# Kernel tuning notes

Measured on AMD Instinct MI355X. Metric: run time of the kernel, lower is better.

The kernel has to match this reference:

```python
import jax
import jax.numpy as jnp
import numpy as np

# ---- static config (matches init_kwargs) ----
V_PATCH_NUMS = [1, 2, 3, 4, 5, 6, 8, 10, 13, 16]
SN = len(V_PATCH_NUMS)
BETA = 0.25
RESI = 0.5          # Phi residual ratio
K_PHI = 4           # share_quant_resi -> PhiPartiallyShared with 4 convs
_ticks = np.linspace(1.0 / 3 / K_PHI, 1 - 1.0 / 3 / K_PHI, K_PHI)  # K==4 branch
PHI_IDX = [int(np.argmin(np.abs(_ticks - si / (SN - 1)))) for si in range(SN)]


def _area_matrix(n_in, n_out):
    """Row-stochastic matrix replicating F.interpolate(mode='area') == adaptive_avg_pool (1D)."""
    M = np.zeros((n_out, n_in), np.float32)
    for i in range(n_out):
        s = (i * n_in) // n_out
        e = -((-(i + 1) * n_in) // n_out)  # ceil
        M[i, s:e] = 1.0 / (e - s)
    return M


def _bicubic_matrix(n_in, n_out):
    """1D bicubic (a=-0.75, align_corners=False, border clamp), matching torch F.interpolate."""
    A = -0.75
    M = np.zeros((n_out, n_in), np.float32)
    scale = n_in / n_out
    for i in range(n_out):
        src = (i + 0.5) * scale - 0.5
        f = int(np.floor(src))
        t = src - f
        for k in range(4):           # taps at f-1 .. f+2
            j = f - 1 + k
            d = abs(src - j)
            if d <= 1.0:
                w = (A + 2) * d ** 3 - (A + 3) * d ** 2 + 1.0
            elif d < 2.0:
                w = A * d ** 3 - 5 * A * d ** 2 + 8 * A * d - 4 * A
            else:
                w = 0.0
            M[i, min(max(j, 0), n_in - 1)] += w
    return M


def _phi(h, w, b):
    # Phi: h*(1-r) + conv3x3(h)*r
    conv = jax.lax.conv_general_dilated(
        h, w, window_strides=(1, 1), padding='SAME',
        dimension_numbers=('NCHW', 'OIHW', 'NCHW')) + b[None, :, None, None]
    return h * (1.0 - RESI) + conv * RESI


def setup_inputs() -> dict:
    key = jax.random.key(0)
    k1, k2, k3 = jax.random.split(key, 3)
    B, C, H = 32, 32, 16
    V = 8192
    f_BChw = jax.random.normal(k1, (B, C, H, H), dtype=jnp.float32)
    emb = jax.random.normal(k2, (V, C), dtype=jnp.float32)
    conv_w = jax.random.normal(k3, (K_PHI, C, C, 3, 3), dtype=jnp.float32) * 0.05
    conv_b = jnp.zeros((K_PHI, C), dtype=jnp.float32)
    return {"f_BChw": f_BChw, "emb": emb, "conv_w": conv_w, "conv_b": conv_b}


def reference(f_BChw, emb, conv_w, conv_b):
    B, C, H, W = f_BChw.shape
    dt = f_BChw.dtype
    f_ng = jax.lax.stop_gradient(f_BChw)
    f_rest = f_ng
    f_hat = jnp.zeros_like(f_ng)
    emb_ng = jax.lax.stop_gradient(emb)     # distances use embedding.weight.data
    emb_sq = jnp.sum(emb_ng ** 2, axis=1)   # [V]
    loss = jnp.zeros((), dt)
    for si, pn in enumerate(V_PATCH_NUMS):
        r = jax.lax.stop_gradient(f_rest)
        if si != SN - 1:
            P = jnp.asarray(_area_matrix(H, pn), dt)
            z = jnp.einsum('ph,bchw,qw->bpqc', P, r, P)   # area pool -> [B,pn,pn,C]
        else:
            z = r.transpose(0, 2, 3, 1)
        z_NC = z.reshape(-1, C)
        d = jnp.sum(z_NC ** 2, axis=1, keepdims=True) + emb_sq - 2.0 * (z_NC @ emb_ng.T)
        idx = jnp.argmin(d, axis=1)                        # [B*pn*pn]
        h = jnp.take(emb, idx, axis=0).reshape(B, pn, pn, C).transpose(0, 3, 1, 2)
        if si != SN - 1:
            U = jnp.asarray(_bicubic_matrix(pn, H), dt)
            h = jnp.einsum('hp,bcpq,wq->bchw', U, h, U)    # bicubic upsample
        pi = PHI_IDX[si]
        h = _phi(h, conv_w[pi], conv_b[pi])
        f_hat = f_hat + h
        f_rest = f_rest - h
        loss = loss + BETA * jnp.mean((jax.lax.stop_gradient(f_hat) - f_BChw) ** 2) \
                    + jnp.mean((f_hat - f_ng) ** 2)
    loss = loss / SN
    f_hat_out = jax.lax.stop_gradient(f_hat) - f_ng + f_BChw   # straight-through
    return f_hat_out, loss
```

## Files before the change

### kernel.cpp

```cpp
#include <hip/hip_runtime.h>
#include <math.h>
#include <stdint.h>

#define B_ 32
#define C_ 32
#define H_ 16
#define V_ 8192
#define HW_ 256
#define NELEM (B_*C_*H_*H_)
#define TBYTES 6208
#define TF4    388

typedef short bf16x8 __attribute__((ext_vector_type(8)));
typedef unsigned short u16x8 __attribute__((ext_vector_type(8)));
typedef float f32x4 __attribute__((ext_vector_type(4)));
typedef unsigned long long ull;

__device__ __forceinline__ unsigned int fkey(float f) {
    unsigned int u = __float_as_uint(f);
    return (u & 0x80000000u) ? ~u : (u | 0x80000000u);
}
__device__ __forceinline__ unsigned short f2bf(float x) {
    unsigned int u = __float_as_uint(x);
    unsigned int r = u + 0x7fffu + ((u >> 16) & 1u);
    return (unsigned short)(r >> 16);
}
__device__ __forceinline__ float bf2f(unsigned short h) {
    return __uint_as_float(((unsigned int)h) << 16);
}

__global__ void __launch_bounds__(256) k_init(
    const float* __restrict__ f, const float* __restrict__ emb,
    float* __restrict__ f_rest, float* __restrict__ f_hat,
    char* __restrict__ blob, float* __restrict__ lossAcc)
{
    int i = blockIdx.x*256 + threadIdx.x;
    if (i < NELEM) { float v = f[i]; f_rest[i] = v; f_hat[i] = 0.f; }
    if (i < 512*64) {
        int t = i >> 6, l = i & 63;
        int row = t*16 + (l & 15);
        int k0 = (l >> 4) * 8;
        const float* er = emb + row*C_ + k0;
        u16x8 h0, h1, h2;
        #pragma unroll
        for (int j = 0; j < 8; ++j) {
            float x = -2.f * er[j];
            unsigned short b0 = f2bf(x);  float r1 = x - bf2f(b0);
            unsigned short b1 = f2bf(r1); float r2 = r1 - bf2f(b1);
            unsigned short b2 = f2bf(r2);
            h0[j] = b0; h1[j] = b1; h2[j] = b2;
        }
        char* tb = blob + (size_t)t*TBYTES;
        *(u16x8*)(tb +        l*16) = h0;
        *(u16x8*)(tb + 2048 + l*16) = h1;
        *(u16x8*)(tb + 4096 + l*16) = h2;
        if ((l >> 4) == 0) {
            const float4* e4 = (const float4*)(emb + row*C_);
            float s = 0.f;
            #pragma unroll
            for (int cc = 0; cc < 8; ++cc) {
                float4 ev = e4[cc];
                s += ev.x*ev.x + ev.y*ev.y + ev.z*ev.z + ev.w*ev.w;
            }
            *(float*)(tb + 6144 + (l & 15)*4) = s;
        }
    }
    if (i == 0) lossAcc[0] = 0.f;
}

__global__ void __launch_bounds__(256) k_pool(
    const float* __restrict__ f_rest, unsigned short* __restrict__ zb,
    ull* __restrict__ best, int pn, int N)
{
    int gid = blockIdx.x*256 + threadIdx.x;
    if (gid >= N*C_) return;
    int c = gid & 31;
    int n = gid >> 5;
    if (c == 0) best[n] = ~0ull;
    int pp = pn*pn;
    int b = n / pp;
    int rem = n - b*pp;
    int p = rem / pn;
    int q = rem - p*pn;
    int hs = (p*H_)/pn,  he = ((p+1)*H_ + pn-1)/pn;
    int ws = (q*H_)/pn,  we = ((q+1)*H_ + pn-1)/pn;
    const float* base = f_rest + ((size_t)(b*C_ + c))*HW_;
    float s = 0.f;
    for (int hh = hs; hh < he; ++hh) {
        #pragma unroll 4
        for (int ww = ws; ww < we; ++ww)
            s += base[hh*H_ + ww];
    }
    float inv = (1.f/(float)(he-hs)) * (1.f/(float)(we-ws));
    float x = s * inv;
    unsigned short b0 = f2bf(x);  float r1 = x - bf2f(b0);
    unsigned short b1 = f2bf(r1); float r2 = r1 - bf2f(b1);
    unsigned short b2 = f2bf(r2);
    size_t o = (size_t)n*C_ + c;
    zb[o]          = b0;
    zb[o + 262144] = b1;
    zb[o + 524288] = b2;
}

__global__ void __launch_bounds__(256) k_vqm(
    const float4* __restrict__ blob, const unsigned short* __restrict__ zb,
    ull* __restrict__ best, int N, int lvs)
{
    __shared__ char chunk[8*TBYTES] __attribute__((aligned(16)));
    int tid = threadIdx.x, lane = tid & 63, w = tid >> 6;
    int qb = blockIdx.x >> lvs;
    int vc = blockIdx.x & ((1 << lvs) - 1);
    int tiles_total = 512 >> lvs;
    int t0 = vc * tiles_total;
    int qt0 = qb*8 + w*2;
    int qr = lane & 15, kq = lane >> 4;

    bf16x8 B00, B01, B02, B10, B11, B12;
    {
        size_t r0 = (size_t)(qt0*16 + qr)*C_ + kq*8;
        size_t r1 = r0 + 16*C_;
        B00 = *(const bf16x8*)(zb + r0);
        B01 = *(const bf16x8*)(zb + r0 + 262144);
        B02 = *(const bf16x8*)(zb + r0 + 524288);
        B10 = *(const bf16x8*)(zb + r1);
        B11 = *(const bf16x8*)(zb + r1 + 262144);
        B12 = *(const bf16x8*)(zb + r1 + 524288);
    }

    float dmin0 = __builtin_inff(), dmin1 = __builtin_inff();
    int imin0 = 0, imin1 = 0;

    for (int tc = 0; tc < tiles_total; tc += 8) {
        int S = (tiles_total - tc) < 8 ? (tiles_total - tc) : 8;
        int cnt = S * TF4;
        __syncthreads();
        const float4* src = blob + (size_t)(t0 + tc)*TF4;
        for (int i = tid; i < cnt; i += 256)
            ((float4*)chunk)[i] = src[i];
        __syncthreads();
        for (int t = 0; t < S; ++t) {
            const char* tb = chunk + t*TBYTES;
            bf16x8 A0 = *(const bf16x8*)(tb +        lane*16);
            bf16x8 A1 = *(const bf16x8*)(tb + 2048 + lane*16);
            bf16x8 A2 = *(const bf16x8*)(tb + 4096 + lane*16);
            f32x4 e2v = *(const f32x4*)(tb + 6144 + kq*16);
            f32x4 a0 = e2v, a1 = e2v;
            #define MF(Af, Bf, Cc) Cc = __builtin_amdgcn_mfma_f32_16x16x32_bf16(Af, Bf, Cc, 0, 0, 0)
            MF(A0, B00, a0); MF(A0, B10, a1);
            MF(A1, B00, a0); MF(A1, B10, a1);
            MF(A0, B01, a0); MF(A0, B11, a1);
            MF(A2, B00, a0); MF(A2, B10, a1);
            MF(A1, B01, a0); MF(A1, B11, a1);
            MF(A0, B02, a0); MF(A0, B12, a1);
            MF(A2, B01, a0); MF(A2, B11, a1);
            MF(A1, B02, a0); MF(A1, B12, a1);
            #undef MF
            int cbase = (t0 + tc + t)*16 + kq*4;
            float mt0 = fminf(fminf(a0.x, a0.y), fminf(a0.z, a0.w));
            if (mt0 < dmin0) {
                dmin0 = mt0;
                imin0 = cbase + ((a0.x==mt0) ? 0 : (a0.y==mt0) ? 1 : (a0.z==mt0) ? 2 : 3);
            }
            float mt1 = fminf(fminf(a1.x, a1.y), fminf(a1.z, a1.w));
            if (mt1 < dmin1) {
                dmin1 = mt1;
                imin1 = cbase + ((a1.x==mt1) ? 0 : (a1.y==mt1) ? 1 : (a1.z==mt1) ? 2 : 3);
            }
        }
    }

    ull k0 = ((ull)fkey(dmin0) << 32) | (unsigned int)imin0;
    ull k1 = ((ull)fkey(dmin1) << 32) | (unsigned int)imin1;
    #pragma unroll
    for (int off = 16; off <= 32; off <<= 1) {
        ull o0 = __shfl_xor(k0, off);
        ull o1 = __shfl_xor(k1, off);
        k0 = o0 < k0 ? o0 : k0;
        k1 = o1 < k1 ? o1 : k1;
    }
    if (kq == 0) {
        int q0 = qt0*16 + qr;
        int q1 = q0 + 16;
        if (q0 < N) atomicMin(best + q0, k0);
        if (q1 < N) atomicMin(best + q1, k1);
    }
}

__device__ __forceinline__ void cubic_taps(int i, int pn, float* wt, int* col) {
    double src = ((double)i + 0.5) * ((double)pn / 16.0) - 0.5;
    double fl = floor(src);
    const double A = -0.75;
    #pragma unroll
    for (int k = 0; k < 4; ++k) {
        double j = fl - 1.0 + (double)k;
        double d = fabs(src - j);
        double w;
        if (d <= 1.0)      w = ((A+2.0)*d - (A+3.0))*d*d + 1.0;
        else if (d < 2.0)  w = ((A*d - 5.0*A)*d + 8.0*A)*d - 4.0*A;
        else               w = 0.0;
        wt[k] = (float)w;
        int jj = (int)j;
        col[k] = jj < 0 ? 0 : (jj > pn-1 ? pn-1 : jj);
    }
}

__global__ void __launch_bounds__(256) k_upphi(
    const ull* __restrict__ best,
    const float* __restrict__ emb,
    const float* __restrict__ cw, const float* __restrict__ cb,
    const float* __restrict__ forig,
    float* __restrict__ f_hat, float* __restrict__ f_rest,
    float* __restrict__ lossAcc, int pn)
{
    __shared__ float hup[16][16][33];
    __shared__ float red[4];
    int bi = blockIdx.x >> 3;
    int g  = blockIdx.x & 7;
    int tid = threadIdx.x;
    int h = tid >> 4, w = tid & 15;

    float wh[4]; int th[4];
    float wwt[4]; int tw[4];
    cubic_taps(h, pn, wh, th);
    cubic_taps(w, pn, wwt, tw);

    float acc[32];
    #pragma unroll
    for (int c = 0; c < 32; ++c) acc[c] = 0.f;
    const ull* bptr = best + bi*pn*pn;
    for (int i = 0; i < 4; ++i) {
        if (wh[i] == 0.f) continue;
        for (int j = 0; j < 4; ++j) {
            float wt = wh[i]*wwt[j];
            if (wt == 0.f) continue;
            unsigned int idx = (unsigned int)(bptr[th[i]*pn + tw[j]] & 0xffffffffull);
            const float4* e4 = (const float4*)(emb + (size_t)idx*C_);
            #pragma unroll
            for (int cc = 0; cc < 8; ++cc) {
                float4 ev = e4[cc];
                acc[cc*4+0] = fmaf(wt, ev.x, acc[cc*4+0]);
                acc[cc*4+1] = fmaf(wt, ev.y, acc[cc*4+1]);
                acc[cc*4+2] = fmaf(wt, ev.z, acc[cc*4+2]);
                acc[cc*4+3] = fmaf(wt, ev.w, acc[cc*4+3]);
            }
        }
    }
    #pragma unroll
    for (int c = 0; c < 32; ++c) hup[h][w][c] = acc[c];
    __syncthreads();

    int co0 = g*4;
    float o4[4];
    #pragma unroll
    for (int k = 0; k < 4; ++k) o4[k] = cb[co0+k];
    for (int ci = 0; ci < 32; ++ci) {
        float hv[9];
        #pragma unroll
        for (int dh = 0; dh < 3; ++dh) {
            int hh = h + dh - 1;
            #pragma unroll
            for (int dw = 0; dw < 3; ++dw) {
                int ww2 = w + dw - 1;
                bool ok = (hh >= 0) & (hh < 16) & (ww2 >= 0) & (ww2 < 16);
                hv[dh*3+dw] = ok ? hup[hh & 15][ww2 & 15][ci] : 0.f;
            }
        }
        #pragma unroll
        for (int k = 0; k < 4; ++k) {
            const float* wr = cw + ((size_t)(co0+k)*C_ + ci)*9;
            float s = 0.f;
            #pragma unroll
            for (int p2 = 0; p2 < 9; ++p2) s = fmaf(hv[p2], wr[p2], s);
            o4[k] += s;
        }
    }

    float sq = 0.f;
    #pragma unroll
    for (int k = 0; k < 4; ++k) {
        float hv0 = hup[h][w][co0+k];
        float outv = 0.5f*hv0 + 0.5f*o4[k];
        size_t off = ((size_t)(bi*C_ + co0 + k))*HW_ + h*16 + w;
        float fh = f_hat[off] + outv;
        f_hat[off] = fh;
        f_rest[off] = f_rest[off] - outv;
        float df = fh - forig[off];
        sq = fmaf(df, df, sq);
    }
    #pragma unroll
    for (int o2 = 32; o2 > 0; o2 >>= 1) sq += __shfl_down(sq, o2, 64);
    if ((tid & 63) == 0) red[tid >> 6] = sq;
    __syncthreads();
    if (tid == 0) atomicAdd(lossAcc, (red[0]+red[1])+(red[2]+red[3]));
}

__global__ void __launch_bounds__(256) k_final(
    const float* __restrict__ f_hat, const float* __restrict__ lossAcc,
    float* __restrict__ out)
{
    int i = blockIdx.x*256 + threadIdx.x;
    if (i < NELEM) out[i] = f_hat[i];
    if (i == 0) out[NELEM] = lossAcc[0] * 1.25f / ((float)NELEM * 10.f);
}

extern "C" void kernel_launch(void* const* d_in, const int* in_sizes, int n_in,
                              void* d_out, int out_size, void* d_ws, size_t ws_size,
                              hipStream_t stream)
{
    const float* f   = (const float*)d_in[0];
    const float* emb = (const float*)d_in[1];
    const float* cw  = (const float*)d_in[2];
    const float* cb  = (const float*)d_in[3];
    float* out = (float*)d_out;
    char* ws = (char*)d_ws;
    ull*   best   = (ull*)ws;
    float* f_rest = (float*)(ws + 65536);
    float* f_hat  = (float*)(ws + 65536 + 1048576);
    unsigned short* zb = (unsigned short*)(ws + 2162688);
    char*  blob   = ws + 3735552;
    float* lossAcc = (float*)(ws + 3735552 + 512*TBYTES);

    volatile double a   = 1.0/3.0/4.0;
    volatile double bb  = 1.0 - a;
    volatile double stp = (bb - a) / 3.0;
    double ticks[4];
    for (int i = 0; i < 4; ++i) { volatile double m = (double)i * stp; ticks[i] = m + a; }
    ticks[3] = bb;
    static const int pns[10] = {1,2,3,4,5,6,8,10,13,16};
    int phi_idx[10];
    for (int si = 0; si < 10; ++si) {
        volatile double x = (double)si / 9.0;
        int bi = 0; double bd = fabs(ticks[0] - x);
        for (int k = 1; k < 4; ++k) {
            double d = fabs(ticks[k] - x);
            if (d < bd) { bd = d; bi = k; }
        }
        phi_idx[si] = bi;
    }

    k_init<<<1024, 256, 0, stream>>>(f, emb, f_rest, f_hat, blob, lossAcc);

    static const int lvss[10] = {7,7,7,7,6,6,5,4,4,3};
    for (int si = 0; si < 10; ++si) {
        int pn = pns[si];
        int N = B_*pn*pn;
        int pthr = N*C_;
        k_pool<<<(pthr+255)/256, 256, 0, stream>>>(f_rest, zb, best, pn, N);
        int qtiles = (N + 127)/128;
        int lvs = lvss[si];
        k_vqm<<<qtiles << lvs, 256, 0, stream>>>((const float4*)blob, zb, best, N, lvs);
        const float* cwp = cw + (size_t)phi_idx[si]*C_*C_*9;
        const float* cbp = cb + (size_t)phi_idx[si]*C_;
        k_upphi<<<B_*8, 256, 0, stream>>>(best, emb, cwp, cbp, f, f_hat, f_rest,
                                          lossAcc, pn);
    }
    k_final<<<1024, 256, 0, stream>>>(f_hat, lossAcc, out);
}
```

Measured before the change: 498.1 us.

## Fuse next-scale pooling into upphi and restructure VQ argmin kernel

The area pooling and bf16 split for the next scale now run at the end of k_upphi, using the freshly updated f_rest held in shared memory. This removes the separate k_pool launch per scale, and ping-pong best buffers let each scale reset the next scale's buffer. k_vqm no longer stages codebook tiles through LDS with barriers; it streams them from global memory with register double-buffering, and each wave now handles 4 query tiles instead of 2. The vocab split factors and launch bounds are retuned to match. In exchange, the kernel relies on cache hits for the codebook reads and uses more registers per wave.

```diff
diff --git a/kernel.cpp b/kernel.cpp
--- a/kernel.cpp
+++ b/kernel.cpp
@@ -9,7 +9,7 @@
 #define HW_ 256
 #define NELEM (B_*C_*H_*H_)
 #define TBYTES 6208
-#define TF4    388
+#define ZPL 262144
 
 typedef short bf16x8 __attribute__((ext_vector_type(8)));
 typedef unsigned short u16x8 __attribute__((ext_vector_type(8)));
@@ -86,103 +86,126 @@
     int ws = (q*H_)/pn,  we = ((q+1)*H_ + pn-1)/pn;
     const float* base = f_rest + ((size_t)(b*C_ + c))*HW_;
     float s = 0.f;
-    for (int hh = hs; hh < he; ++hh) {
-        #pragma unroll 4
+    for (int hh = hs; hh < he; ++hh)
         for (int ww = ws; ww < we; ++ww)
             s += base[hh*H_ + ww];
-    }
     float inv = (1.f/(float)(he-hs)) * (1.f/(float)(we-ws));
     float x = s * inv;
     unsigned short b0 = f2bf(x);  float r1 = x - bf2f(b0);
     unsigned short b1 = f2bf(r1); float r2 = r1 - bf2f(b1);
     unsigned short b2 = f2bf(r2);
     size_t o = (size_t)n*C_ + c;
-    zb[o]          = b0;
-    zb[o + 262144] = b1;
-    zb[o + 524288] = b2;
-}
-
-__global__ void __launch_bounds__(256) k_vqm(
-    const float4* __restrict__ blob, const unsigned short* __restrict__ zb,
+    zb[o] = b0; zb[o + ZPL] = b1; zb[o + 2*ZPL] = b2;
+}
+
+__device__ __forceinline__ void qstep(
+    const bf16x8 a0, const bf16x8 a1, const bf16x8 a2, const f32x4 e2v,
+    const bf16x8* Bf, int cbase, float& dmin, int& imin)
+{
+    f32x4 acc = e2v;
+    acc = __builtin_amdgcn_mfma_f32_16x16x32_bf16(a0, Bf[0], acc, 0, 0, 0);
+    acc = __builtin_amdgcn_mfma_f32_16x16x32_bf16(a1, Bf[0], acc, 0, 0, 0);
+    acc = __builtin_amdgcn_mfma_f32_16x16x32_bf16(a0, Bf[1], acc, 0, 0, 0);
+    acc = __builtin_amdgcn_mfma_f32_16x16x32_bf16(a2, Bf[0], acc, 0, 0, 0);
+    acc = __builtin_amdgcn_mfma_f32_16x16x32_bf16(a1, Bf[1], acc, 0, 0, 0);
+    acc = __builtin_amdgcn_mfma_f32_16x16x32_bf16(a0, Bf[2], acc, 0, 0, 0);
+    float mt = fminf(fminf(acc.x, acc.y), fminf(acc.z, acc.w));
+    if (mt < dmin) {
+        dmin = mt;
+        imin = cbase + ((acc.x==mt) ? 0 : (acc.y==mt) ? 1 : (acc.z==mt) ? 2 : 3);
+    }
+}
+
+__global__ void __launch_bounds__(256, 2) k_vqm(
+    const char* __restrict__ blob, const unsigned short* __restrict__ zb,
     ull* __restrict__ best, int N, int lvs)
 {
-    __shared__ char chunk[8*TBYTES] __attribute__((aligned(16)));
     int tid = threadIdx.x, lane = tid & 63, w = tid >> 6;
+    int qtiles_total = N >> 4;
     int qb = blockIdx.x >> lvs;
     int vc = blockIdx.x & ((1 << lvs) - 1);
-    int tiles_total = 512 >> lvs;
-    int t0 = vc * tiles_total;
-    int qt0 = qb*8 + w*2;
+    int tiles = 512 >> lvs;
+    int t0 = vc * tiles;
+    int qt0 = qb*16 + w*4;
     int qr = lane & 15, kq = lane >> 4;
 
-    bf16x8 B00, B01, B02, B10, B11, B12;
+    bf16x8 Bf0[3], Bf1[3], Bf2[3], Bf3[3];
+    int qv0, qv1, qv2, qv3;
     {
-        size_t r0 = (size_t)(qt0*16 + qr)*C_ + kq*8;
-        size_t r1 = r0 + 16*C_;
-        B00 = *(const bf16x8*)(zb + r0);
-        B01 = *(const bf16x8*)(zb + r0 + 262144);
-        B02 = *(const bf16x8*)(zb + r0 + 524288);
-        B10 = *(const bf16x8*)(zb + r1);
-        B11 = *(const bf16x8*)(zb + r1 + 262144);
-        B12 = *(const bf16x8*)(zb + r1 + 524288);
-    }
-
-    float dmin0 = __builtin_inff(), dmin1 = __builtin_inff();
-    int imin0 = 0, imin1 = 0;
-
-    for (int tc = 0; tc < tiles_total; tc += 8) {
-        int S = (tiles_total - tc) < 8 ? (tiles_total - tc) : 8;
-        int cnt = S * TF4;
-        __syncthreads();
-        const float4* src = blob + (size_t)(t0 + tc)*TF4;
-        for (int i = tid; i < cnt; i += 256)
-            ((float4*)chunk)[i] = src[i];
-        __syncthreads();
-        for (int t = 0; t < S; ++t) {
-            const char* tb = chunk + t*TBYTES;
-            bf16x8 A0 = *(const bf16x8*)(tb +        lane*16);
-            bf16x8 A1 = *(const bf16x8*)(tb + 2048 + lane*16);
-            bf16x8 A2 = *(const bf16x8*)(tb + 4096 + lane*16);
-            f32x4 e2v = *(const f32x4*)(tb + 6144 + kq*16);
-            f32x4 a0 = e2v, a1 = e2v;
-            #define MF(Af, Bf, Cc) Cc = __builtin_amdgcn_mfma_f32_16x16x32_bf16(Af, Bf, Cc, 0, 0, 0)
-            MF(A0, B00, a0); MF(A0, B10, a1);
-            MF(A1, B00, a0); MF(A1, B10, a1);
-            MF(A0, B01, a0); MF(A0, B11, a1);
-            MF(A2, B00, a0); MF(A2, B10, a1);
-            MF(A1, B01, a0); MF(A1, B11, a1);
-            MF(A0, B02, a0); MF(A0, B12, a1);
-            MF(A2, B01, a0); MF(A2, B11, a1);
-            MF(A1, B02, a0); MF(A1, B12, a1);
-            #undef MF
-            int cbase = (t0 + tc + t)*16 + kq*4;
-            float mt0 = fminf(fminf(a0.x, a0.y), fminf(a0.z, a0.w));
-            if (mt0 < dmin0) {
-                dmin0 = mt0;
-                imin0 = cbase + ((a0.x==mt0) ? 0 : (a0.y==mt0) ? 1 : (a0.z==mt0) ? 2 : 3);
-            }
-            float mt1 = fminf(fminf(a1.x, a1.y), fminf(a1.z, a1.w));
-            if (mt1 < dmin1) {
-                dmin1 = mt1;
-                imin1 = cbase + ((a1.x==mt1) ? 0 : (a1.y==mt1) ? 1 : (a1.z==mt1) ? 2 : 3);
-            }
-        }
-    }
-
-    ull k0 = ((ull)fkey(dmin0) << 32) | (unsigned int)imin0;
-    ull k1 = ((ull)fkey(dmin1) << 32) | (unsigned int)imin1;
-    #pragma unroll
-    for (int off = 16; off <= 32; off <<= 1) {
-        ull o0 = __shfl_xor(k0, off);
-        ull o1 = __shfl_xor(k1, off);
-        k0 = o0 < k0 ? o0 : k0;
-        k1 = o1 < k1 ? o1 : k1;
-    }
-    if (kq == 0) {
-        int q0 = qt0*16 + qr;
-        int q1 = q0 + 16;
-        if (q0 < N) atomicMin(best + q0, k0);
-        if (q1 < N) atomicMin(best + q1, k1);
+        int qtj;
+        size_t o;
+        qtj = qt0 + 0; qv0 = (qtj < qtiles_total);
+        o = (size_t)((qv0 ? qtj : 0)*16 + qr)*C_ + kq*8;
+        Bf0[0] = *(const bf16x8*)(zb + o);
+        Bf0[1] = *(const bf16x8*)(zb + o + ZPL);
+        Bf0[2] = *(const bf16x8*)(zb + o + 2*ZPL);
+        qtj = qt0 + 1; qv1 = (qtj < qtiles_total);
+        o = (size_t)((qv1 ? qtj : 0)*16 + qr)*C_ + kq*8;
+        Bf1[0] = *(const bf16x8*)(zb + o);
+        Bf1[1] = *(const bf16x8*)(zb + o + ZPL);
+        Bf1[2] = *(const bf16x8*)(zb + o + 2*ZPL);
+        qtj = qt0 + 2; qv2 = (qtj < qtiles_total);
+        o = (size_t)((qv2 ? qtj : 0)*16 + qr)*C_ + kq*8;
+        Bf2[0] = *(const bf16x8*)(zb + o);
+        Bf2[1] = *(const bf16x8*)(zb + o + ZPL);
+        Bf2[2] = *(const bf16x8*)(zb + o + 2*ZPL);
+        qtj = qt0 + 3; qv3 = (qtj < qtiles_total);
+        o = (size_t)((qv3 ? qtj : 0)*16 + qr)*C_ + kq*8;
+        Bf3[0] = *(const bf16x8*)(zb + o);
+        Bf3[1] = *(const bf16x8*)(zb + o + ZPL);
+        Bf3[2] = *(const bf16x8*)(zb + o + 2*ZPL);
+    }
+
+    float dmin[4]; int imin[4];
+    #pragma unroll
+    for (int j = 0; j < 4; ++j) { dmin[j] = __builtin_inff(); imin[j] = 0; }
+
+    const char* tb = blob + (size_t)t0*TBYTES;
+    bf16x8 Xa0, Xa1, Xa2; f32x4 Xe;
+    bf16x8 Ya0, Ya1, Ya2; f32x4 Ye;
+    Xa0 = *(const bf16x8*)(tb +        lane*16);
+    Xa1 = *(const bf16x8*)(tb + 2048 + lane*16);
+    Xa2 = *(const bf16x8*)(tb + 4096 + lane*16);
+    Xe  = *(const f32x4*)(tb + 6144 + kq*16);
+
+    for (int tt = 0; tt < tiles; tt += 2) {
+        const char* nb = tb + TBYTES;
+        Ya0 = *(const bf16x8*)(nb +        lane*16);
+        Ya1 = *(const bf16x8*)(nb + 2048 + lane*16);
+        Ya2 = *(const bf16x8*)(nb + 4096 + lane*16);
+        Ye  = *(const f32x4*)(nb + 6144 + kq*16);
+        {
+            int cbase = (t0 + tt)*16 + kq*4;
+            qstep(Xa0, Xa1, Xa2, Xe, Bf0, cbase, dmin[0], imin[0]);
+            qstep(Xa0, Xa1, Xa2, Xe, Bf1, cbase, dmin[1], imin[1]);
+            qstep(Xa0, Xa1, Xa2, Xe, Bf2, cbase, dmin[2], imin[2]);
+            qstep(Xa0, Xa1, Xa2, Xe, Bf3, cbase, dmin[3], imin[3]);
+        }
+        const char* nb2 = (tt + 2 < tiles) ? tb + 2*TBYTES : tb;
+        Xa0 = *(const bf16x8*)(nb2 +        lane*16);
+        Xa1 = *(const bf16x8*)(nb2 + 2048 + lane*16);
+        Xa2 = *(const bf16x8*)(nb2 + 4096 + lane*16);
+        Xe  = *(const f32x4*)(nb2 + 6144 + kq*16);
+        {
+            int cbase = (t0 + tt + 1)*16 + kq*4;
+            qstep(Ya0, Ya1, Ya2, Ye, Bf0, cbase, dmin[0], imin[0]);
+            qstep(Ya0, Ya1, Ya2, Ye, Bf1, cbase, dmin[1], imin[1]);
+            qstep(Ya0, Ya1, Ya2, Ye, Bf2, cbase, dmin[2], imin[2]);
+            qstep(Ya0, Ya1, Ya2, Ye, Bf3, cbase, dmin[3], imin[3]);
+        }
+        tb += 2*TBYTES;
+    }
+
+    int qvv[4] = {qv0, qv1, qv2, qv3};
+    #pragma unroll
+    for (int j = 0; j < 4; ++j) {
+        ull key = ((ull)fkey(dmin[j]) << 32) | (unsigned int)imin[j];
+        ull o1 = __shfl_xor(key, 16); key = o1 < key ? o1 : key;
+        ull o2 = __shfl_xor(key, 32); key = o2 < key ? o2 : key;
+        if (kq == 0 && qvv[j]) {
+            int q = (qt0 + j)*16 + qr;
+            atomicMin(best + q, key);
+        }
     }
 }
 
@@ -210,7 +233,8 @@
     const float* __restrict__ cw, const float* __restrict__ cb,
     const float* __restrict__ forig,
     float* __restrict__ f_hat, float* __restrict__ f_rest,
-    float* __restrict__ lossAcc, int pn)
+    float* __restrict__ lossAcc, int pn,
+    int pn2, unsigned short* __restrict__ zb, ull* __restrict__ bestN)
 {
     __shared__ float hup[16][16][33];
     __shared__ float red[4];
@@ -274,6 +298,7 @@
             o4[k] += s;
         }
     }
+    __syncthreads();
 
     float sq = 0.f;
     #pragma unroll
@@ -283,7 +308,9 @@
         size_t off = ((size_t)(bi*C_ + co0 + k))*HW_ + h*16 + w;
         float fh = f_hat[off] + outv;
         f_hat[off] = fh;
-        f_rest[off] = f_rest[off] - outv;
+        float fr = f_rest[off] - outv;
+        f_rest[off] = fr;
+        hup[h][w][co0+k] = fr;
         float df = fh - forig[off];
         sq = fmaf(df, df, sq);
     }
@@ -292,6 +319,27 @@
     if ((tid & 63) == 0) red[tid >> 6] = sq;
     __syncthreads();
     if (tid == 0) atomicAdd(lossAcc, (red[0]+red[1])+(red[2]+red[3]));
+
+    if (pn2 > 0 && h < pn2 && w < pn2) {
+        int hs = (h*H_)/pn2,  he2 = ((h+1)*H_ + pn2-1)/pn2;
+        int ws2 = (w*H_)/pn2, we2 = ((w+1)*H_ + pn2-1)/pn2;
+        float inv = (1.f/(float)(he2-hs)) * (1.f/(float)(we2-ws2));
+        int n = bi*pn2*pn2 + h*pn2 + w;
+        #pragma unroll
+        for (int k = 0; k < 4; ++k) {
+            float s = 0.f;
+            for (int hh = hs; hh < he2; ++hh)
+                for (int ww = ws2; ww < we2; ++ww)
+                    s += hup[hh][ww][co0+k];
+            float x = s * inv;
+            unsigned short b0 = f2bf(x);  float r1 = x - bf2f(b0);
+            unsigned short b1 = f2bf(r1); float r2 = r1 - bf2f(b1);
+            unsigned short b2 = f2bf(r2);
+            size_t o = (size_t)n*C_ + co0 + k;
+            zb[o] = b0; zb[o + ZPL] = b1; zb[o + 2*ZPL] = b2;
+        }
+        if (g == 0) bestN[n] = ~0ull;
+    }
 }
 
 __global__ void __launch_bounds__(256) k_final(
@@ -313,12 +361,13 @@
     const float* cb  = (const float*)d_in[3];
     float* out = (float*)d_out;
     char* ws = (char*)d_ws;
-    ull*   best   = (ull*)ws;
-    float* f_rest = (float*)(ws + 65536);
-    float* f_hat  = (float*)(ws + 65536 + 1048576);
-    unsigned short* zb = (unsigned short*)(ws + 2162688);
-    char*  blob   = ws + 3735552;
-    float* lossAcc = (float*)(ws + 3735552 + 512*TBYTES);
+    ull*   best0  = (ull*)ws;
+    ull*   best1  = (ull*)(ws + 65536);
+    float* f_rest = (float*)(ws + 131072);
+    float* f_hat  = (float*)(ws + 131072 + 1048576);
+    unsigned short* zb = (unsigned short*)(ws + 2228224);
+    char*  blob   = ws + 3801088;
+    float* lossAcc = (float*)(ws + 6979584);
 
     volatile double a   = 1.0/3.0/4.0;
     volatile double bb  = 1.0 - a;
@@ -339,20 +388,23 @@
     }
 
     k_init<<<1024, 256, 0, stream>>>(f, emb, f_rest, f_hat, blob, lossAcc);
-
-    static const int lvss[10] = {7,7,7,7,6,6,5,4,4,3};
+    k_pool<<<4, 256, 0, stream>>>(f_rest, zb, best0, 1, 32);
+
+    static const int lvss[10] = {6,6,6,6,6,6,6,5,5,4};
     for (int si = 0; si < 10; ++si) {
         int pn = pns[si];
         int N = B_*pn*pn;
-        int pthr = N*C_;
-        k_pool<<<(pthr+255)/256, 256, 0, stream>>>(f_rest, zb, best, pn, N);
-        int qtiles = (N + 127)/128;
+        int qtiles = N >> 4;
+        int qblocks = (qtiles + 15)/16;
         int lvs = lvss[si];
-        k_vqm<<<qtiles << lvs, 256, 0, stream>>>((const float4*)blob, zb, best, N, lvs);
+        ull* bcur  = (si & 1) ? best1 : best0;
+        ull* bnext = (si & 1) ? best0 : best1;
+        k_vqm<<<qblocks << lvs, 256, 0, stream>>>(blob, zb, bcur, N, lvs);
         const float* cwp = cw + (size_t)phi_idx[si]*C_*C_*9;
         const float* cbp = cb + (size_t)phi_idx[si]*C_;
-        k_upphi<<<B_*8, 256, 0, stream>>>(best, emb, cwp, cbp, f, f_hat, f_rest,
-                                          lossAcc, pn);
+        int pn2 = (si < 9) ? pns[si+1] : 0;
+        k_upphi<<<B_*8, 256, 0, stream>>>(bcur, emb, cwp, cbp, f, f_hat, f_rest,
+                                          lossAcc, pn, pn2, zb, bnext);
     }
     k_final<<<1024, 256, 0, stream>>>(f_hat, lossAcc, out);
 }
```

After: 437.1 us. 12.3% less time.
